# Performance work log

Measured on AMD Instinct MI355X. Metric: run time of the kernel, lower is better.

The kernel has to match this reference:

```python
import jax, jax.numpy as jnp
import numpy as np

N_NODES = 100000
N_EDGES = 1600000
IN_DIM = 128
HID = 64
OUT_DIM = 3


def _glorot(key, shape):
    fan_in, fan_out = shape[0], shape[1]
    std = (2.0 / (fan_in + fan_out)) ** 0.5
    return jax.random.normal(key, shape, jnp.float32) * std


def setup_inputs() -> dict:
    key = jax.random.key(0)
    ks = jax.random.split(key, 12)
    x = jax.random.normal(ks[0], (N_NODES, IN_DIM), jnp.float32)
    edge_index = jax.random.randint(ks[1], (2, N_EDGES), 0, N_NODES, dtype=jnp.int32)
    return {
        "x": x,
        "edge_index": edge_index,
        "W1": _glorot(ks[2], (IN_DIM, HID)), "b1": jnp.zeros((HID,), jnp.float32),
        "W2": _glorot(ks[3], (HID, HID)), "b2": jnp.zeros((HID,), jnp.float32),
        "W3": _glorot(ks[4], (HID, HID)), "b3": jnp.zeros((HID,), jnp.float32),
        "W4": _glorot(ks[5], (HID, HID // 2)), "b4": jnp.zeros((HID // 2,), jnp.float32),
        "Wh": _glorot(ks[6], (HID // 2, OUT_DIM)), "bh": jnp.zeros((OUT_DIM,), jnp.float32),
    }


def reference(x, edge_index, W1, b1, W2, b2, W3, b3, W4, b4, Wh, bh):
    n = x.shape[0]
    self_loops = jnp.arange(n, dtype=edge_index.dtype)
    src = jnp.concatenate([edge_index[0], self_loops])  # message sources j
    dst = jnp.concatenate([edge_index[1], self_loops])  # aggregation targets i
    # symmetric GCN normalization with self-loops: deg over targets (unit edge weights)
    deg = jax.ops.segment_sum(jnp.ones_like(dst, jnp.float32), dst, num_segments=n)
    dinv = jnp.where(deg > 0, jax.lax.rsqrt(deg), 0.0)
    norm = dinv[src] * dinv[dst]  # [E+N]

    def gcn(h, W, b):
        h = h @ W  # transform first (PyG GCNConv order)
        agg = jax.ops.segment_sum(h[src] * norm[:, None], dst, num_segments=n)
        return agg + b

    h = jax.nn.relu(gcn(x, W1, b1))   # dropout is identity in eval mode
    h = jax.nn.relu(gcn(h, W2, b2))
    h = jax.nn.relu(gcn(h, W3, b3))
    h = jax.nn.relu(gcn(h, W4, b4))
    return h @ Wh + bh  # [N, 3]
```

## Files before the change

kernel.cpp:

```cpp
#include <hip/hip_runtime.h>
#include <hip/hip_bf16.h>
#include <hip/hip_fp16.h>
#include <cstdint>


#define MAXD 512
#define EB   8192
#define PADSLACK 2048

typedef _Float16 half8v __attribute__((ext_vector_type(8)));
typedef _Float16 half2v __attribute__((ext_vector_type(2)));
typedef float    float4v __attribute__((ext_vector_type(4)));

#if defined(__has_builtin)
#if __has_builtin(__builtin_amdgcn_fdot2)
#define HAVE_FDOT2 1
#endif
#endif

__device__ __forceinline__ float fdot2f(half2v a, half2v b, float c) {
#ifdef HAVE_FDOT2
    return __builtin_amdgcn_fdot2(a, b, c, false);
#else
    return c + (float)a[0] * (float)b[0] + (float)a[1] * (float)b[1];
#endif
}

__device__ __forceinline__ void digit_base_scan(const int* __restrict__ totals,
                                                int ND, int* pairs, int* cbs) {
    const int t = threadIdx.x;
    const int e0 = 2 * t, e1 = 2 * t + 1;
    int v0 = (e0 < ND) ? totals[e0] : 0;
    int v1 = (e1 < ND) ? totals[e1] : 0;
    pairs[t] = v0 + v1;
    __syncthreads();
    for (int off = 1; off < 256; off <<= 1) {
        int x = (t >= off) ? pairs[t - off] : 0;
        __syncthreads();
        pairs[t] += x;
        __syncthreads();
    }
    int ep = pairs[t] - v0 - v1;
    cbs[e0] = ep;
    cbs[e1] = ep + v0;
    __syncthreads();
}

__device__ __forceinline__ void hist_body(const int* __restrict__ ei,
                                          int* __restrict__ histM, int E, int b) {
    __shared__ int hist[MAXD];
    const int tid = threadIdx.x;
    hist[tid] = 0; hist[tid + 256] = 0;
    __syncthreads();
    const int base = b * EB;
#pragma unroll 2
    for (int it = 0; it < EB / 256; it += 4) {
        int d[4]; bool ok[4];
#pragma unroll
        for (int u = 0; u < 4; ++u) {
            int e = base + (it + u) * 256 + tid;
            ok[u] = e < E;
            d[u] = ok[u] ? ei[E + e] : 0;
        }
#pragma unroll
        for (int u = 0; u < 4; ++u)
            if (ok[u]) atomicAdd(&hist[d[u] >> 8], 1);
    }
    __syncthreads();
    histM[(size_t)b * MAXD + tid] = hist[tid];
    histM[(size_t)b * MAXD + tid + 256] = hist[tid + 256];
}

__global__ __launch_bounds__(256) void scan_digits_k(int* __restrict__ histM,
                                                     int* __restrict__ totals,
                                                     int NBLK) {
    __shared__ int s[256];
    const int t = threadIdx.x, dg = blockIdx.x;
    int v = (t < NBLK) ? histM[(size_t)t * MAXD + dg] : 0;
    s[t] = v;
    __syncthreads();
    for (int off = 1; off < 256; off <<= 1) {
        int x = (t >= off) ? s[t - off] : 0;
        __syncthreads();
        s[t] += x;
        __syncthreads();
    }
    if (t < NBLK) histM[(size_t)t * MAXD + dg] = s[t] - v;
    if (t == 255) totals[dg] = s[255];
}

template <int K, int OUT>
__device__ __forceinline__ void gemm_body(const float* __restrict__ H,
                                          const float* __restrict__ W,
                                          float* __restrict__ Tout, int n, int bx) {
    constexpr int TX  = OUT / 4;
    constexpr int TY  = 256 / TX;
    constexpr int BM  = TY * 4;
    constexpr int BK  = 32;
    constexpr int PAD = 4;

    __shared__ float At[BK][BM + PAD];
    __shared__ float Ws[BK][OUT];

    const int t    = threadIdx.x;
    const int cx   = t % TX;
    const int ry   = t / TX;
    const int row0 = bx * BM;

    float acc[4][4] = {{0.f}};
    const int arow = t >> 3;
    const int af4  = t & 7;

    for (int k0 = 0; k0 < K; k0 += BK) {
#pragma unroll
        for (int p = 0; p < BM / 32; ++p) {
            int r  = arow + p * 32;
            int gr = row0 + r;
            int grc = gr < n ? gr : n - 1;
            float4 v = *reinterpret_cast<const float4*>(
                H + (size_t)grc * K + k0 + af4 * 4);
            At[af4 * 4 + 0][r] = v.x;
            At[af4 * 4 + 1][r] = v.y;
            At[af4 * 4 + 2][r] = v.z;
            At[af4 * 4 + 3][r] = v.w;
        }
#pragma unroll
        for (int p = 0; p < (BK * OUT) / 1024; ++p) {
            int idx = t + p * 256;
            int wk  = idx / (OUT / 4);
            int wf  = idx % (OUT / 4);
            float4 v = *reinterpret_cast<const float4*>(
                W + (size_t)(k0 + wk) * OUT + wf * 4);
            *reinterpret_cast<float4*>(&Ws[wk][wf * 4]) = v;
        }
        __syncthreads();
#pragma unroll
        for (int k = 0; k < BK; ++k) {
            float4 a = *reinterpret_cast<const float4*>(&At[k][ry * 4]);
            float4 w = *reinterpret_cast<const float4*>(&Ws[k][cx * 4]);
            acc[0][0] = fmaf(a.x, w.x, acc[0][0]);
            acc[0][1] = fmaf(a.x, w.y, acc[0][1]);
            acc[0][2] = fmaf(a.x, w.z, acc[0][2]);
            acc[0][3] = fmaf(a.x, w.w, acc[0][3]);
            acc[1][0] = fmaf(a.y, w.x, acc[1][0]);
            acc[1][1] = fmaf(a.y, w.y, acc[1][1]);
            acc[1][2] = fmaf(a.y, w.z, acc[1][2]);
            acc[1][3] = fmaf(a.y, w.w, acc[1][3]);
            acc[2][0] = fmaf(a.z, w.x, acc[2][0]);
            acc[2][1] = fmaf(a.z, w.y, acc[2][1]);
            acc[2][2] = fmaf(a.z, w.z, acc[2][2]);
            acc[2][3] = fmaf(a.z, w.w, acc[2][3]);
            acc[3][0] = fmaf(a.w, w.x, acc[3][0]);
            acc[3][1] = fmaf(a.w, w.y, acc[3][1]);
            acc[3][2] = fmaf(a.w, w.z, acc[3][2]);
            acc[3][3] = fmaf(a.w, w.w, acc[3][3]);
        }
        __syncthreads();
    }
#pragma unroll
    for (int i = 0; i < 4; ++i) {
        int gr = row0 + ry * 4 + i;
        if (gr < n) {
            float4 v = make_float4(acc[i][0], acc[i][1], acc[i][2], acc[i][3]);
            *reinterpret_cast<float4*>(Tout + (size_t)gr * OUT + cx * 4) = v;
        }
    }
}

__device__ __forceinline__ void pack_body(const int* __restrict__ ei,
                                          const int* __restrict__ histM,
                                          const int* __restrict__ totals,
                                          int* __restrict__ packed,
                                          int E, int ND, int b) {
    __shared__ int pairs[256];
    __shared__ int cbs[MAXD];
    __shared__ int cur[MAXD];
    const int tid = threadIdx.x;
    digit_base_scan(totals, ND, pairs, cbs);
    for (int t = tid; t < ND; t += 256)
        cur[t] = cbs[t] + histM[(size_t)b * MAXD + t];
    __syncthreads();
    const int base = b * EB;
    for (int it = 0; it < EB / 256; it += 4) {
        int s[4], d[4]; bool ok[4];
#pragma unroll
        for (int u = 0; u < 4; ++u) {
            int e = base + (it + u) * 256 + tid;
            ok[u] = e < E;
            if (ok[u]) { s[u] = ei[e]; d[u] = ei[E + e]; }
        }
#pragma unroll
        for (int u = 0; u < 4; ++u) {
            if (ok[u]) {
                int pos = atomicAdd(&cur[d[u] >> 8], 1);
                packed[pos] = (s[u] << 8) | (d[u] & 255);
            }
        }
    }
}

__global__ __launch_bounds__(256) void hist_gemm1_k(
    const int* __restrict__ ei, int* __restrict__ histM, int E,
    const float* __restrict__ x, const float* __restrict__ W1,
    float* __restrict__ T1, int n, int NH) {
    const int bx = blockIdx.x;
    if (bx < NH) hist_body(ei, histM, E, bx);
    else         gemm_body<128, 64>(x, W1, T1, n, bx - NH);
}

__global__ __launch_bounds__(256) void pack_gemm1_k(
    const int* __restrict__ ei, const int* __restrict__ histM,
    const int* __restrict__ totals, int* __restrict__ packed,
    const float* __restrict__ x, const float* __restrict__ W1,
    float* __restrict__ T1, int n, int E, int ND, int NPB, int G1) {
    const int bx = blockIdx.x;
    if (bx < NPB) pack_body(ei, histM, totals, packed, E, ND, bx);
    else          gemm_body<128, 64>(x, W1, T1, n, G1 + bx - NPB);
}

__global__ __launch_bounds__(256) void bucket_k(const int* __restrict__ packed,
                                                const int* __restrict__ totals,
                                                int ND,
                                                int* __restrict__ col,
                                                int4* __restrict__ rpc,
                                                float* __restrict__ dinv,
                                                const float* __restrict__ Traw,
                                                __half* __restrict__ Th, int n) {
    __shared__ int   pairs[256];
    __shared__ int   cbs[MAXD];
    __shared__ int   hist[256];
    __shared__ int   pref[256];
    __shared__ int   cur[256];
    __shared__ float dinv_l[256];

    const int tid = threadIdx.x;
    const int dg  = blockIdx.x;
    digit_base_scan(totals, ND, pairs, cbs);
    const int base  = cbs[dg];
    const int m     = totals[dg];
    const int basep = base + dg * PADSLACK;

    hist[tid] = 0;
    __syncthreads();
    for (int k0 = 0; k0 < m; k0 += 1024) {
        int v[4]; bool ok[4];
#pragma unroll
        for (int u = 0; u < 4; ++u) {
            int k = k0 + u * 256 + tid;
            ok[u] = k < m;
            v[u] = ok[u] ? packed[base + k] : 0;
        }
#pragma unroll
        for (int u = 0; u < 4; ++u)
            if (ok[u]) atomicAdd(&hist[v[u] & 255], 1);
    }
    __syncthreads();
    const int deg   = hist[tid];
    const int cnt_p = (deg + 8) & ~7;
    pref[tid] = cnt_p;
    __syncthreads();
    for (int off = 1; off < 256; off <<= 1) {
        int x = (tid >= off) ? pref[tid - off] : 0;
        __syncthreads();
        pref[tid] += x;
        __syncthreads();
    }
    const int rp = basep + pref[tid] - cnt_p;
    const float di = rsqrtf((float)(deg + 1));
    dinv_l[tid] = di;
    cur[tid] = rp + 1;
    const int d = dg * 256 + tid;
    if (d < n) {
        rpc[d]  = make_int4(rp, cnt_p, __float_as_int(di), 0);
        dinv[d] = di;
        col[rp] = d;
        for (int k = deg + 1; k < cnt_p; ++k) col[rp + k] = n;
    }
    __syncthreads();
    for (int k0 = 0; k0 < m; k0 += 1024) {
        int v[4]; bool ok[4];
#pragma unroll
        for (int u = 0; u < 4; ++u) {
            int k = k0 + u * 256 + tid;
            ok[u] = k < m;
            v[u] = ok[u] ? packed[base + k] : 0;
        }
#pragma unroll
        for (int u = 0; u < 4; ++u) {
            if (ok[u]) {
                int pos = atomicAdd(&cur[v[u] & 255], 1);
                col[pos] = v[u] >> 8;
            }
        }
    }
    const int r0 = dg * 256;
#pragma unroll 4
    for (int it = 0; it < 16; ++it) {
        int idx = it * 256 + tid;
        int rl  = idx >> 4;
        int r   = r0 + rl;
        if (r < n) {
            float4 v = reinterpret_cast<const float4*>(Traw)[(size_t)r * 16 + (idx & 15)];
            float dd = dinv_l[rl];
            union { ushort4 u; __half h[4]; } pk;
            pk.h[0] = __float2half_rn(v.x * dd);
            pk.h[1] = __float2half_rn(v.y * dd);
            pk.h[2] = __float2half_rn(v.z * dd);
            pk.h[3] = __float2half_rn(v.w * dd);
            reinterpret_cast<ushort4*>(Th)[(size_t)r * 16 + (idx & 15)] = pk.u;
        }
    }
    if (dg == 0 && tid < 16) {
        uint2 z; z.x = 0u; z.y = 0u;
        reinterpret_cast<uint2*>(Th)[(size_t)n * 16 + tid] = z;
    }
}

template <int OUT>
__global__ __launch_bounds__(256) void gemm_mfma_k(
    const _Float16* __restrict__ H, const float* __restrict__ W,
    const float* __restrict__ dinv, _Float16* __restrict__ T, int n) {
    constexpr int NT = OUT / 16;
    const int lane = threadIdx.x & 63;
    const int m16  = lane & 15;
    const int quad = lane >> 4;
    const int wid  = (blockIdx.x * blockDim.x + threadIdx.x) >> 6;
    const int nw   = (gridDim.x * blockDim.x) >> 6;

    half8v bfrag[NT][2];
#pragma unroll
    for (int t = 0; t < NT; ++t)
#pragma unroll
        for (int h = 0; h < 2; ++h)
#pragma unroll
            for (int j = 0; j < 8; ++j)
                bfrag[t][h][j] = (_Float16)W[(size_t)(h * 32 + quad * 8 + j) * OUT
                                             + t * 16 + m16];

    const int nblk = (n + 15) >> 4;
    for (int rb = wid; rb < nblk; rb += nw) {
        const int r0 = rb * 16;
        int ra = r0 + m16; if (ra >= n) ra = n - 1;
        const half8v* hrow = reinterpret_cast<const half8v*>(H + (size_t)ra * 64);
        half8v a0 = hrow[quad];
        half8v a1 = hrow[4 + quad];

        float4v dfr[NT];
#pragma unroll
        for (int t = 0; t < NT; ++t) {
            float4v z = {0.f, 0.f, 0.f, 0.f};
            z = __builtin_amdgcn_mfma_f32_16x16x32_f16(a0, bfrag[t][0], z, 0, 0, 0);
            z = __builtin_amdgcn_mfma_f32_16x16x32_f16(a1, bfrag[t][1], z, 0, 0, 0);
            dfr[t] = z;
        }
#pragma unroll
        for (int reg = 0; reg < 4; ++reg) {
            int row = r0 + quad * 4 + reg;
            if (row < n) {
                float di = dinv[row];
#pragma unroll
                for (int t = 0; t < NT; ++t)
                    T[(size_t)row * 64 + t * 16 + m16] =
                        (_Float16)(dfr[t][reg] * di);
            }
        }
    }
}

template <int NB, int LR>
__device__ __forceinline__ void gather_issue(int c_l, const uint2* __restrict__ T2,
                                             int q, int sw, uint2* __restrict__ v) {
    constexpr int NSW = 64 / LR;
    constexpr int GPE = 8 / NSW;
#pragma unroll
    for (int g = 0; g < NB; ++g)
#pragma unroll
        for (int u = 0; u < GPE; ++u) {
            int cc = __shfl(c_l, g * 8 + u * NSW + sw, 64);
            v[g * GPE + u] = T2[(size_t)cc * 16 + q];
        }
}

template <int NG, int LR>
__device__ __forceinline__ void gather_fdot(const uint2* __restrict__ v, float4& acc) {
    constexpr int NSW = 64 / LR;
    constexpr int GPE = 8 / NSW;
    constexpr int NV  = NG * GPE;
    const half2v s10 = {(_Float16)1.f, (_Float16)0.f};
    const half2v s01 = {(_Float16)0.f, (_Float16)1.f};
#pragma unroll
    for (int k = 0; k < NV; ++k) {
        union { uint2 uu; half2v h[2]; } cv; cv.uu = v[k];
        acc.x = fdot2f(cv.h[0], s10, acc.x);
        acc.y = fdot2f(cv.h[0], s01, acc.y);
        acc.z = fdot2f(cv.h[1], s10, acc.z);
        acc.w = fdot2f(cv.h[1], s01, acc.w);
    }
}

template <int NB, int LR>
__device__ __forceinline__ void gather_batch(int c_l, const uint2* __restrict__ T2,
                                             int q, int sw, float4& acc, int g0) {
    constexpr int NSW = 64 / LR;
    constexpr int GPE = 8 / NSW;
    constexpr int NV  = NB * GPE;
    const half2v s10 = {(_Float16)1.f, (_Float16)0.f};
    const half2v s01 = {(_Float16)0.f, (_Float16)1.f};
    uint2 v[NV];
#pragma unroll
    for (int g = 0; g < NB; ++g)
#pragma unroll
        for (int u = 0; u < GPE; ++u) {
            int cc = __shfl(c_l, (g0 + g) * 8 + u * NSW + sw, 64);
            v[g * GPE + u] = T2[(size_t)cc * 16 + q];
        }
#pragma unroll
    for (int k = 0; k < NV; ++k) {
        union { uint2 uu; half2v h[2]; } cv; cv.uu = v[k];
        acc.x = fdot2f(cv.h[0], s10, acc.x);
        acc.y = fdot2f(cv.h[0], s01, acc.y);
        acc.z = fdot2f(cv.h[1], s10, acc.z);
        acc.w = fdot2f(cv.h[1], s01, acc.w);
    }
}

template <int LR, bool FUSE_HEAD>
__device__ __forceinline__ void agg_body(
    int i, int n, int nw, int lane, int q, int sw,
    const uint2* __restrict__ T2, const int* __restrict__ col,
    const int4* __restrict__ rpc,
    int4& rcP, int4& rcQ, int4& rcR, int& cP, int& cQ,
    uint2* __restrict__ vP, uint2* __restrict__ vQ,
    const float4& b4, void* __restrict__ O,
    const float* __restrict__ Wh, const float* __restrict__ bh) {
    int iS = i + 3 * nw; if (iS >= n) iS = n - 1;
    int4 rcS = rpc[iS];
    int cR = col[rcR.x + lane];
    {
        int ng = rcQ.y >> 3; if (ng > 4) ng = 4;
        switch (ng) {
            case 1: gather_issue<1, LR>(cQ, T2, q, sw, vQ); break;
            case 2: gather_issue<2, LR>(cQ, T2, q, sw, vQ); break;
            case 3: gather_issue<3, LR>(cQ, T2, q, sw, vQ); break;
            default: gather_issue<4, LR>(cQ, T2, q, sw, vQ); break;
        }
    }
    const int   cnt = rcP.y;
    const float di  = __int_as_float(rcP.z);
    float4 acc = make_float4(0.f, 0.f, 0.f, 0.f);
    switch (cnt >> 3) {
        case 1: gather_fdot<1, LR>(vP, acc); break;
        case 2: gather_fdot<2, LR>(vP, acc); break;
        case 3: gather_fdot<3, LR>(vP, acc); break;
        case 4: gather_fdot<4, LR>(vP, acc); break;
        case 5: gather_fdot<4, LR>(vP, acc); gather_batch<1, LR>(cP, T2, q, sw, acc, 4); break;
        case 6: gather_fdot<4, LR>(vP, acc); gather_batch<2, LR>(cP, T2, q, sw, acc, 4); break;
        case 7: gather_fdot<4, LR>(vP, acc); gather_batch<3, LR>(cP, T2, q, sw, acc, 4); break;
        default: {
            gather_fdot<4, LR>(vP, acc);
            gather_batch<4, LR>(cP, T2, q, sw, acc, 4);
            const int start = rcP.x;
            for (int base = 64; base < cnt; base += 64) {
                int m = cnt - base; if (m > 64) m = 64;
                int c_l = col[start + base + lane];
                for (int jg = 0; jg < m; jg += 32) {
                    int nb2 = (m - jg) >> 3; if (nb2 > 4) nb2 = 4;
                    int g0 = jg >> 3;
                    switch (nb2) {
                        case 1: gather_batch<1, LR>(c_l, T2, q, sw, acc, g0); break;
                        case 2: gather_batch<2, LR>(c_l, T2, q, sw, acc, g0); break;
                        case 3: gather_batch<3, LR>(c_l, T2, q, sw, acc, g0); break;
                        default: gather_batch<4, LR>(c_l, T2, q, sw, acc, g0); break;
                    }
                }
            }
            break;
        }
    }
#pragma unroll
    for (int off = LR; off < 64; off <<= 1) {
        acc.x += __shfl_xor(acc.x, off, 64);
        acc.y += __shfl_xor(acc.y, off, 64);
        acc.z += __shfl_xor(acc.z, off, 64);
        acc.w += __shfl_xor(acc.w, off, 64);
    }
    float4 h;
    h.x = fmaxf(fmaf(di, acc.x, b4.x), 0.f);
    h.y = fmaxf(fmaf(di, acc.y, b4.y), 0.f);
    h.z = fmaxf(fmaf(di, acc.z, b4.z), 0.f);
    h.w = fmaxf(fmaf(di, acc.w, b4.w), 0.f);
    if constexpr (!FUSE_HEAD) {
        if (sw == 0) {
            union { ushort4 u; __half hh[4]; } pk;
            pk.hh[0] = __float2half_rn(h.x);
            pk.hh[1] = __float2half_rn(h.y);
            pk.hh[2] = __float2half_rn(h.z);
            pk.hh[3] = __float2half_rn(h.w);
            ushort* base_p = (ushort*)O + (size_t)i * 64;
            *reinterpret_cast<ushort4*>(base_p + 4 * q) = pk.u;
        }
    } else {
        float* Of = (float*)O;
        float p0 = h.x * Wh[(4 * q + 0) * 3 + 0];
        float p1 = h.x * Wh[(4 * q + 0) * 3 + 1];
        float p2 = h.x * Wh[(4 * q + 0) * 3 + 2];
        p0 = fmaf(h.y, Wh[(4 * q + 1) * 3 + 0], p0);
        p1 = fmaf(h.y, Wh[(4 * q + 1) * 3 + 1], p1);
        p2 = fmaf(h.y, Wh[(4 * q + 1) * 3 + 2], p2);
        p0 = fmaf(h.z, Wh[(4 * q + 2) * 3 + 0], p0);
        p1 = fmaf(h.z, Wh[(4 * q + 2) * 3 + 1], p1);
        p2 = fmaf(h.z, Wh[(4 * q + 2) * 3 + 2], p2);
        p0 = fmaf(h.w, Wh[(4 * q + 3) * 3 + 0], p0);
        p1 = fmaf(h.w, Wh[(4 * q + 3) * 3 + 1], p1);
        p2 = fmaf(h.w, Wh[(4 * q + 3) * 3 + 2], p2);
#pragma unroll
        for (int off = 1; off < LR; off <<= 1) {
            p0 += __shfl_xor(p0, off, 64);
            p1 += __shfl_xor(p1, off, 64);
            p2 += __shfl_xor(p2, off, 64);
        }
        if (lane == 0) {
            Of[(size_t)i * 3 + 0] = p0 + bh[0];
            Of[(size_t)i * 3 + 1] = p1 + bh[1];
            Of[(size_t)i * 3 + 2] = p2 + bh[2];
        }
    }
    rcP = rcQ; rcQ = rcR; rcR = rcS;
    cP = cQ; cQ = cR;
}

template <int LR, bool FUSE_HEAD>
__global__ __launch_bounds__(256, 4) void agg_k(const __half* __restrict__ T,
                                             const int4* __restrict__ rpc,
                                             const int* __restrict__ col,
                                             const float* __restrict__ bias,
                                             void* __restrict__ O, int n,
                                             const float* __restrict__ Wh,
                                             const float* __restrict__ bh) {
    constexpr int NSW = 64 / LR;
    constexpr int GPE = 8 / NSW;
    constexpr int NV  = 4 * GPE;
    const int lane = threadIdx.x & 63;
    const int q    = lane % LR;
    const int sw   = lane / LR;
    const int wid  = (blockIdx.x * blockDim.x + threadIdx.x) >> 6;
    const int nw   = (gridDim.x * blockDim.x) >> 6;
    if (wid >= n) return;

    const uint2* __restrict__ T2 = reinterpret_cast<const uint2*>(T);
    const float4 b4 = reinterpret_cast<const float4*>(bias)[q];

    int i1 = wid + nw;     if (i1 >= n) i1 = n - 1;
    int i2 = wid + 2 * nw; if (i2 >= n) i2 = n - 1;
    int4 rcP = rpc[wid];
    int4 rcQ = rpc[i1];
    int4 rcR = rpc[i2];
    int  cP  = col[rcP.x + lane];
    int  cQ  = col[rcQ.x + lane];

    uint2 vA[NV], vB[NV];
#pragma unroll
    for (int k = 0; k < NV; ++k) { vA[k] = make_uint2(0u, 0u); vB[k] = make_uint2(0u, 0u); }
    {
        int ng = rcP.y >> 3; if (ng > 4) ng = 4;
        switch (ng) {
            case 1: gather_issue<1, LR>(cP, T2, q, sw, vA); break;
            case 2: gather_issue<2, LR>(cP, T2, q, sw, vA); break;
            case 3: gather_issue<3, LR>(cP, T2, q, sw, vA); break;
            default: gather_issue<4, LR>(cP, T2, q, sw, vA); break;
        }
    }
    for (int i = wid; i < n; i += 2 * nw) {
        agg_body<LR, FUSE_HEAD>(i, n, nw, lane, q, sw, T2, col, rpc,
                                rcP, rcQ, rcR, cP, cQ, vA, vB, b4, O, Wh, bh);
        if (i + nw < n)
            agg_body<LR, FUSE_HEAD>(i + nw, n, nw, lane, q, sw, T2, col, rpc,
                                    rcP, rcQ, rcR, cP, cQ, vB, vA, b4, O, Wh, bh);
    }
}

extern "C" void kernel_launch(void* const* d_in, const int* in_sizes, int n_in,
                              void* d_out, int out_size, void* d_ws, size_t ws_size,
                              hipStream_t stream) {
    const float* x  = (const float*)d_in[0];
    const int*   ei = (const int*)d_in[1];
    const float* W1 = (const float*)d_in[2];
    const float* b1 = (const float*)d_in[3];
    const float* W2 = (const float*)d_in[4];
    const float* b2 = (const float*)d_in[5];
    const float* W3 = (const float*)d_in[6];
    const float* b3 = (const float*)d_in[7];
    const float* W4 = (const float*)d_in[8];
    const float* b4 = (const float*)d_in[9];
    const float* Wh = (const float*)d_in[10];
    const float* bh = (const float*)d_in[11];
    float* out = (float*)d_out;

    const int n = in_sizes[0] / 128;
    const int E = in_sizes[1] / 2;
    const int ND   = (n + 255) / 256;
    const int NBLK = (E + EB - 1) / EB;

    char* ws = (char*)d_ws;
    auto alloc = [&](size_t bytes) {
        char* p = ws;
        ws += (bytes + 255) & ~(size_t)255;
        return p;
    };
    int*    histM  = (int*)alloc((size_t)NBLK * MAXD * 4);
    int*    totals = (int*)alloc((size_t)MAXD * 4);
    int*    packed = (int*)alloc((size_t)E * 4);
    int*    col    = (int*)alloc(((size_t)E + (size_t)ND * PADSLACK + 256) * 4);
    int4*   rpc    = (int4*)alloc((size_t)n * 16);
    float*  dinv   = (float*)alloc((size_t)n * 4);
    float*  bufF   = (float*)alloc((size_t)n * 64 * 4);
    __half* bufH   = (__half*)alloc(((size_t)n + 1) * 64 * 2);
    __half* bufG   = (__half*)bufF;

    dim3 blk(256);
    const int G  = (n + 63) / 64;
    const int G1 = G / 3;
    const int G2 = G - G1;
    const int agg_blocks = 2048;
    const int mfma_blocks = 640;

    hist_gemm1_k<<<dim3(NBLK + G1), blk, 0, stream>>>(ei, histM, E, x, W1, bufF, n, NBLK);
    scan_digits_k<<<dim3(ND), blk, 0, stream>>>(histM, totals, NBLK);
    pack_gemm1_k<<<dim3(NBLK + G2), blk, 0, stream>>>(ei, histM, totals, packed,
                                                      x, W1, bufF, n, E, ND, NBLK, G1);
    bucket_k<<<dim3(ND), blk, 0, stream>>>(packed, totals, ND, col, rpc,
                                           dinv, bufF, bufH, n);
    agg_k<16, false><<<dim3(agg_blocks), blk, 0, stream>>>(
        bufH, rpc, col, b1, bufG, n, nullptr, nullptr);
    gemm_mfma_k<64><<<dim3(mfma_blocks), blk, 0, stream>>>(
        (const _Float16*)bufG, W2, dinv, (_Float16*)bufH, n);
    agg_k<16, false><<<dim3(agg_blocks), blk, 0, stream>>>(
        bufH, rpc, col, b2, bufG, n, nullptr, nullptr);
    gemm_mfma_k<64><<<dim3(mfma_blocks), blk, 0, stream>>>(
        (const _Float16*)bufG, W3, dinv, (_Float16*)bufH, n);
    agg_k<16, false><<<dim3(agg_blocks), blk, 0, stream>>>(
        bufH, rpc, col, b3, bufG, n, nullptr, nullptr);
    gemm_mfma_k<32><<<dim3(mfma_blocks), blk, 0, stream>>>(
        (const _Float16*)bufG, W4, dinv, (_Float16*)bufH, n);
    agg_k<8, true><<<dim3(agg_blocks), blk, 0, stream>>>(
        bufH, rpc, col, b4, out, n, Wh, bh);
}
```

Before: 348.3 us.

## Pad CSR rows to 32 and use fixed 32-neighbor gather batches

Pads each node's adjacency row to a multiple of 32 instead of 8 and aligns bucket bases, so the aggregation kernel always issues a fixed 4-group prefetch and loops in 32-wide chunks without degree-based switch dispatch. Head weights are hoisted into registers once per thread, and the launch bounds occupancy hint is raised from 4 to 6. The intent is to cut branch divergence and code size and to raise occupancy. In exchange, padding adds more dummy gathers for low-degree nodes (average degree about 17), which means more memory traffic, and a larger slack region is needed.

```diff
diff --git a/kernel.cpp b/kernel.cpp
--- a/kernel.cpp
+++ b/kernel.cpp
@@ -6,7 +6,7 @@
 
 #define MAXD 512
 #define EB   8192
-#define PADSLACK 2048
+#define PADSLACK 8224
 
 typedef _Float16 half8v __attribute__((ext_vector_type(8)));
 typedef _Float16 half2v __attribute__((ext_vector_type(2)));
@@ -238,7 +238,7 @@
     digit_base_scan(totals, ND, pairs, cbs);
     const int base  = cbs[dg];
     const int m     = totals[dg];
-    const int basep = base + dg * PADSLACK;
+    const int basep = ((base + 31) & ~31) + dg * PADSLACK;
 
     hist[tid] = 0;
     __syncthreads();
@@ -256,7 +256,7 @@
     }
     __syncthreads();
     const int deg   = hist[tid];
-    const int cnt_p = (deg + 8) & ~7;
+    const int cnt_p = (deg + 32) & ~31;
     pref[tid] = cnt_p;
     __syncthreads();
     for (int off = 1; off < 256; off <<= 1) {
@@ -367,13 +367,13 @@
     }
 }
 
-template <int NB, int LR>
-__device__ __forceinline__ void gather_issue(int c_l, const uint2* __restrict__ T2,
-                                             int q, int sw, uint2* __restrict__ v) {
+template <int LR>
+__device__ __forceinline__ void gather_issue4(int c_l, const uint2* __restrict__ T2,
+                                              int q, int sw, uint2* __restrict__ v) {
     constexpr int NSW = 64 / LR;
     constexpr int GPE = 8 / NSW;
 #pragma unroll
-    for (int g = 0; g < NB; ++g)
+    for (int g = 0; g < 4; ++g)
 #pragma unroll
         for (int u = 0; u < GPE; ++u) {
             int cc = __shfl(c_l, g * 8 + u * NSW + sw, 64);
@@ -381,11 +381,11 @@
         }
 }
 
-template <int NG, int LR>
-__device__ __forceinline__ void gather_fdot(const uint2* __restrict__ v, float4& acc) {
+template <int LR>
+__device__ __forceinline__ void gather_fdot4(const uint2* __restrict__ v, float4& acc) {
     constexpr int NSW = 64 / LR;
     constexpr int GPE = 8 / NSW;
-    constexpr int NV  = NG * GPE;
+    constexpr int NV  = 4 * GPE;
     const half2v s10 = {(_Float16)1.f, (_Float16)0.f};
     const half2v s01 = {(_Float16)0.f, (_Float16)1.f};
 #pragma unroll
@@ -398,30 +398,13 @@
     }
 }
 
-template <int NB, int LR>
-__device__ __forceinline__ void gather_batch(int c_l, const uint2* __restrict__ T2,
-                                             int q, int sw, float4& acc, int g0) {
-    constexpr int NSW = 64 / LR;
-    constexpr int GPE = 8 / NSW;
-    constexpr int NV  = NB * GPE;
-    const half2v s10 = {(_Float16)1.f, (_Float16)0.f};
-    const half2v s01 = {(_Float16)0.f, (_Float16)1.f};
-    uint2 v[NV];
-#pragma unroll
-    for (int g = 0; g < NB; ++g)
-#pragma unroll
-        for (int u = 0; u < GPE; ++u) {
-            int cc = __shfl(c_l, (g0 + g) * 8 + u * NSW + sw, 64);
-            v[g * GPE + u] = T2[(size_t)cc * 16 + q];
-        }
-#pragma unroll
-    for (int k = 0; k < NV; ++k) {
-        union { uint2 uu; half2v h[2]; } cv; cv.uu = v[k];
-        acc.x = fdot2f(cv.h[0], s10, acc.x);
-        acc.y = fdot2f(cv.h[0], s01, acc.y);
-        acc.z = fdot2f(cv.h[1], s10, acc.z);
-        acc.w = fdot2f(cv.h[1], s01, acc.w);
-    }
+template <int LR>
+__device__ __forceinline__ void gather_sync4(int c_l, const uint2* __restrict__ T2,
+                                             int q, int sw, float4& acc) {
+    constexpr int GPE = 8 / (64 / LR);
+    uint2 v[4 * GPE];
+    gather_issue4<LR>(c_l, T2, q, sw, v);
+    gather_fdot4<LR>(v, acc);
 }
 
 template <int LR, bool FUSE_HEAD>
@@ -429,52 +412,22 @@
     int i, int n, int nw, int lane, int q, int sw,
     const uint2* __restrict__ T2, const int* __restrict__ col,
     const int4* __restrict__ rpc,
-    int4& rcP, int4& rcQ, int4& rcR, int& cP, int& cQ,
+    int4& rcP, int4& rcQ, int4& rcR, int& cQ,
     uint2* __restrict__ vP, uint2* __restrict__ vQ,
-    const float4& b4, void* __restrict__ O,
-    const float* __restrict__ Wh, const float* __restrict__ bh) {
+    const float4& b4, const float* __restrict__ wh, float bh0, float bh1, float bh2,
+    void* __restrict__ O) {
     int iS = i + 3 * nw; if (iS >= n) iS = n - 1;
     int4 rcS = rpc[iS];
-    int cR = col[rcR.x + lane];
-    {
-        int ng = rcQ.y >> 3; if (ng > 4) ng = 4;
-        switch (ng) {
-            case 1: gather_issue<1, LR>(cQ, T2, q, sw, vQ); break;
-            case 2: gather_issue<2, LR>(cQ, T2, q, sw, vQ); break;
-            case 3: gather_issue<3, LR>(cQ, T2, q, sw, vQ); break;
-            default: gather_issue<4, LR>(cQ, T2, q, sw, vQ); break;
-        }
-    }
+    int cR = col[rcR.x + (lane & 31)];
+    gather_issue4<LR>(cQ, T2, q, sw, vQ);
     const int   cnt = rcP.y;
     const float di  = __int_as_float(rcP.z);
     float4 acc = make_float4(0.f, 0.f, 0.f, 0.f);
-    switch (cnt >> 3) {
-        case 1: gather_fdot<1, LR>(vP, acc); break;
-        case 2: gather_fdot<2, LR>(vP, acc); break;
-        case 3: gather_fdot<3, LR>(vP, acc); break;
-        case 4: gather_fdot<4, LR>(vP, acc); break;
-        case 5: gather_fdot<4, LR>(vP, acc); gather_batch<1, LR>(cP, T2, q, sw, acc, 4); break;
-        case 6: gather_fdot<4, LR>(vP, acc); gather_batch<2, LR>(cP, T2, q, sw, acc, 4); break;
-        case 7: gather_fdot<4, LR>(vP, acc); gather_batch<3, LR>(cP, T2, q, sw, acc, 4); break;
-        default: {
-            gather_fdot<4, LR>(vP, acc);
-            gather_batch<4, LR>(cP, T2, q, sw, acc, 4);
-            const int start = rcP.x;
-            for (int base = 64; base < cnt; base += 64) {
-                int m = cnt - base; if (m > 64) m = 64;
-                int c_l = col[start + base + lane];
-                for (int jg = 0; jg < m; jg += 32) {
-                    int nb2 = (m - jg) >> 3; if (nb2 > 4) nb2 = 4;
-                    int g0 = jg >> 3;
-                    switch (nb2) {
-                        case 1: gather_batch<1, LR>(c_l, T2, q, sw, acc, g0); break;
-                        case 2: gather_batch<2, LR>(c_l, T2, q, sw, acc, g0); break;
-                        case 3: gather_batch<3, LR>(c_l, T2, q, sw, acc, g0); break;
-                        default: gather_batch<4, LR>(c_l, T2, q, sw, acc, g0); break;
-                    }
-                }
-            }
-            break;
+    gather_fdot4<LR>(vP, acc);
+    if (cnt > 32) {
+        for (int s0 = 32; s0 < cnt; s0 += 32) {
+            int c_l = col[rcP.x + s0 + (lane & 31)];
+            gather_sync4<LR>(c_l, T2, q, sw, acc);
         }
     }
 #pragma unroll
@@ -501,18 +454,18 @@
         }
     } else {
         float* Of = (float*)O;
-        float p0 = h.x * Wh[(4 * q + 0) * 3 + 0];
-        float p1 = h.x * Wh[(4 * q + 0) * 3 + 1];
-        float p2 = h.x * Wh[(4 * q + 0) * 3 + 2];
-        p0 = fmaf(h.y, Wh[(4 * q + 1) * 3 + 0], p0);
-        p1 = fmaf(h.y, Wh[(4 * q + 1) * 3 + 1], p1);
-        p2 = fmaf(h.y, Wh[(4 * q + 1) * 3 + 2], p2);
-        p0 = fmaf(h.z, Wh[(4 * q + 2) * 3 + 0], p0);
-        p1 = fmaf(h.z, Wh[(4 * q + 2) * 3 + 1], p1);
-        p2 = fmaf(h.z, Wh[(4 * q + 2) * 3 + 2], p2);
-        p0 = fmaf(h.w, Wh[(4 * q + 3) * 3 + 0], p0);
-        p1 = fmaf(h.w, Wh[(4 * q + 3) * 3 + 1], p1);
-        p2 = fmaf(h.w, Wh[(4 * q + 3) * 3 + 2], p2);
+        float p0 = h.x * wh[0];
+        float p1 = h.x * wh[1];
+        float p2 = h.x * wh[2];
+        p0 = fmaf(h.y, wh[3], p0);
+        p1 = fmaf(h.y, wh[4], p1);
+        p2 = fmaf(h.y, wh[5], p2);
+        p0 = fmaf(h.z, wh[6], p0);
+        p1 = fmaf(h.z, wh[7], p1);
+        p2 = fmaf(h.z, wh[8], p2);
+        p0 = fmaf(h.w, wh[9], p0);
+        p1 = fmaf(h.w, wh[10], p1);
+        p2 = fmaf(h.w, wh[11], p2);
 #pragma unroll
         for (int off = 1; off < LR; off <<= 1) {
             p0 += __shfl_xor(p0, off, 64);
@@ -520,17 +473,17 @@
             p2 += __shfl_xor(p2, off, 64);
         }
         if (lane == 0) {
-            Of[(size_t)i * 3 + 0] = p0 + bh[0];
-            Of[(size_t)i * 3 + 1] = p1 + bh[1];
-            Of[(size_t)i * 3 + 2] = p2 + bh[2];
+            Of[(size_t)i * 3 + 0] = p0 + bh0;
+            Of[(size_t)i * 3 + 1] = p1 + bh1;
+            Of[(size_t)i * 3 + 2] = p2 + bh2;
         }
     }
     rcP = rcQ; rcQ = rcR; rcR = rcS;
-    cP = cQ; cQ = cR;
+    cQ = cR;
 }
 
 template <int LR, bool FUSE_HEAD>
-__global__ __launch_bounds__(256, 4) void agg_k(const __half* __restrict__ T,
+__global__ __launch_bounds__(256, 6) void agg_k(const __half* __restrict__ T,
                                              const int4* __restrict__ rpc,
                                              const int* __restrict__ col,
                                              const float* __restrict__ bias,
@@ -549,33 +502,35 @@
 
     const uint2* __restrict__ T2 = reinterpret_cast<const uint2*>(T);
     const float4 b4 = reinterpret_cast<const float4*>(bias)[q];
+    float wh[12]; float bh0 = 0.f, bh1 = 0.f, bh2 = 0.f;
+    if constexpr (FUSE_HEAD) {
+#pragma unroll
+        for (int j = 0; j < 4; ++j)
+#pragma unroll
+            for (int c = 0; c < 3; ++c)
+                wh[j * 3 + c] = Wh[(4 * q + j) * 3 + c];
+        bh0 = bh[0]; bh1 = bh[1]; bh2 = bh[2];
+    }
 
     int i1 = wid + nw;     if (i1 >= n) i1 = n - 1;
     int i2 = wid + 2 * nw; if (i2 >= n) i2 = n - 1;
     int4 rcP = rpc[wid];
     int4 rcQ = rpc[i1];
     int4 rcR = rpc[i2];
-    int  cP  = col[rcP.x + lane];
-    int  cQ  = col[rcQ.x + lane];
+    int  c0  = col[rcP.x + (lane & 31)];
+    int  cQ  = col[rcQ.x + (lane & 31)];
 
     uint2 vA[NV], vB[NV];
-#pragma unroll
-    for (int k = 0; k < NV; ++k) { vA[k] = make_uint2(0u, 0u); vB[k] = make_uint2(0u, 0u); }
-    {
-        int ng = rcP.y >> 3; if (ng > 4) ng = 4;
-        switch (ng) {
-            case 1: gather_issue<1, LR>(cP, T2, q, sw, vA); break;
-            case 2: gather_issue<2, LR>(cP, T2, q, sw, vA); break;
-            case 3: gather_issue<3, LR>(cP, T2, q, sw, vA); break;
-            default: gather_issue<4, LR>(cP, T2, q, sw, vA); break;
-        }
-    }
+    gather_issue4<LR>(c0, T2, q, sw, vA);
+
     for (int i = wid; i < n; i += 2 * nw) {
         agg_body<LR, FUSE_HEAD>(i, n, nw, lane, q, sw, T2, col, rpc,
-                                rcP, rcQ, rcR, cP, cQ, vA, vB, b4, O, Wh, bh);
+                                rcP, rcQ, rcR, cQ, vA, vB,
+                                b4, wh, bh0, bh1, bh2, O);
         if (i + nw < n)
             agg_body<LR, FUSE_HEAD>(i + nw, n, nw, lane, q, sw, T2, col, rpc,
-                                    rcP, rcQ, rcR, cP, cQ, vB, vA, b4, O, Wh, bh);
+                                    rcP, rcQ, rcR, cQ, vB, vA,
+                                    b4, wh, bh0, bh1, bh2, O);
     }
 }
 
```

Measured after the change: 386.1 us. 1.11x slower.
